# Kernel tuning notes

Measured on AMD Instinct MI355X. Metric: run time of the kernel, lower is better.

The kernel has to match this reference:

```python
import jax, jax.numpy as jnp
import numpy as np

N_NODES = 150000
N_EDGES = 4800000
IN_FEAT = 64
HID = 16
N_GRAPHS = 512
EDGE_DIM = 2


def setup_inputs() -> dict:
    key = jax.random.key(0)
    ks = jax.random.split(key, 32)
    g = lambda i, shape, scale=0.1: jax.random.normal(ks[i], shape, dtype=jnp.float32) * scale
    inp = {
        'x': jax.random.normal(ks[0], (N_NODES, IN_FEAT), dtype=jnp.float32),
        'edge_index': jax.random.randint(ks[1], (2, N_EDGES), 0, N_NODES),
        'edge_attr': jax.random.normal(ks[2], (N_EDGES, EDGE_DIM), dtype=jnp.float32),
        'batch': jnp.sort(jax.random.randint(ks[3], (N_NODES,), 0, N_GRAPHS)),
        # GATConv 1
        'W1': g(4, (IN_FEAT, HID)), 'We1': g(5, (EDGE_DIM, HID)),
        'att_src1': g(6, (HID,)), 'att_dst1': g(7, (HID,)), 'att_edge1': g(8, (HID,)),
        'b1': g(9, (HID,)),
        'bn1_g': jnp.ones((HID,), jnp.float32), 'bn1_b': jnp.zeros((HID,), jnp.float32),
        # GATConv 2
        'W2': g(10, (HID, HID)), 'We2': g(11, (EDGE_DIM, HID)),
        'att_src2': g(12, (HID,)), 'att_dst2': g(13, (HID,)), 'att_edge2': g(14, (HID,)),
        'b2': g(15, (HID,)),
        # D2RL head
        'bnl1_g': jnp.ones((HID,), jnp.float32), 'bnl1_b': jnp.zeros((HID,), jnp.float32),
        'Wl1': g(16, (HID, HID)), 'bl1': g(17, (HID,)),
        'bnl2_g': jnp.ones((2 * HID,), jnp.float32), 'bnl2_b': jnp.zeros((2 * HID,), jnp.float32),
        'Wl2': g(18, (2 * HID, HID)), 'bl2': g(19, (HID,)),
        'bnl3_g': jnp.ones((2 * HID,), jnp.float32), 'bnl3_b': jnp.zeros((2 * HID,), jnp.float32),
        'Wl3': g(20, (2 * HID, HID)), 'bl3': g(21, (HID,)),
        'Wo': g(22, (HID, 1)), 'bo': g(23, (1,)),
    }
    return inp


def _bn(x, gamma, beta, eps=1e-5):
    mu = x.mean(0)
    var = x.var(0)  # biased, matches torch BN training-mode normalization
    return gamma * (x - mu) * jax.lax.rsqrt(var + eps) + beta


def _gat(x, src, dst, edge_attr, W, We, a_s, a_d, a_e, bias, n):
    h = x @ W                                   # [N, HID]
    alpha_s = h @ a_s                           # [N]
    alpha_d = h @ a_d                           # [N]
    alpha_e = (edge_attr @ We) @ a_e            # [E]
    # add self-loops; self-loop edge_attr = mean of incoming edge_attr (PyG fill_value='mean')
    cnt = jax.ops.segment_sum(jnp.ones(src.shape[0], x.dtype), dst, num_segments=n)
    loop_attr = jax.ops.segment_sum(edge_attr, dst, num_segments=n) / jnp.maximum(cnt, 1.0)[:, None]
    loop_alpha_e = (loop_attr @ We) @ a_e       # [N]
    idx = jnp.arange(n)
    src_f = jnp.concatenate([src, idx])
    dst_f = jnp.concatenate([dst, idx])
    logits = jax.nn.leaky_relu(alpha_s[src_f] + alpha_d[dst_f]
                               + jnp.concatenate([alpha_e, loop_alpha_e]), 0.2)
    # segment softmax over destination neighborhoods
    m = jax.ops.segment_max(logits, dst_f, num_segments=n)
    ex = jnp.exp(logits - m[dst_f])
    denom = jax.ops.segment_sum(ex, dst_f, num_segments=n)
    alpha = ex / (denom[dst_f] + 1e-16)
    out = jax.ops.segment_sum(alpha[:, None] * h[src_f], dst_f, num_segments=n)
    return out + bias


def reference(x, edge_index, edge_attr, batch,
              W1, We1, att_src1, att_dst1, att_edge1, b1, bn1_g, bn1_b,
              W2, We2, att_src2, att_dst2, att_edge2, b2,
              bnl1_g, bnl1_b, Wl1, bl1,
              bnl2_g, bnl2_b, Wl2, bl2,
              bnl3_g, bnl3_b, Wl3, bl3,
              Wo, bo):
    n = x.shape[0]
    src, dst = edge_index[0], edge_index[1]
    h = jax.nn.relu(_gat(x, src, dst, edge_attr, W1, We1, att_src1, att_dst1, att_edge1, b1, n))
    h = _bn(h, bn1_g, bn1_b)
    h = jax.nn.relu(_gat(h, src, dst, edge_attr, W2, We2, att_src2, att_dst2, att_edge2, b2, n))
    # mean aggregation per graph
    gcnt = jax.ops.segment_sum(jnp.ones(n, h.dtype), batch, num_segments=N_GRAPHS, indices_are_sorted=True)
    pooled = jax.ops.segment_sum(h, batch, num_segments=N_GRAPHS, indices_are_sorted=True) / jnp.maximum(gcnt, 1.0)[:, None]
    z = jax.nn.relu(_bn(pooled, bnl1_g, bnl1_b) @ Wl1 + bl1)
    z = jax.nn.relu(_bn(jnp.concatenate([z, pooled], axis=1), bnl2_g, bnl2_b) @ Wl2 + bl2)
    z = jax.nn.relu(_bn(jnp.concatenate([z, pooled], axis=1), bnl3_g, bnl3_b) @ Wl3 + bl3)
    return z @ Wo + bo
```

## Files before the change

### kernel.cpp

```cpp
#include <hip/hip_runtime.h>
#include <hip/hip_fp16.h>
#include <math.h>

#define H 16
#define NF 64
#define TPB 256
#define NB 256
#define NBSHIFT 8
#define BTPB 1024
#define NSHIFT 6
#define MAXB 2560
#define SBLK 256
#define SITEMS 16
#define SRCMASK 0x3FFFF
#define CAP 3072
#define STAGE_CAP 18752
#define PSPAN 96

__device__ __forceinline__ float lrelu(float v){ return v > 0.f ? v : 0.2f*v; }

__global__ void k_prep(const float* __restrict__ We1, const float* __restrict__ ae1,
                       const float* __restrict__ We2, const float* __restrict__ ae2,
                       float* __restrict__ params){
  int t = threadIdx.x;
  if (t < 4){
    const float* We = (t < 2) ? We1 : We2;
    const float* ae = (t < 2) ? ae1 : ae2;
    int r = t & 1;
    float s = 0.f;
    for (int c = 0; c < H; ++c) s += We[r*H + c] * ae[c];
    params[t] = s;
  }
}

__global__ __launch_bounds__(BTPB) void k_bcount(const int* __restrict__ dst,
    int* __restrict__ cnt, int E, int B, int chunk){
  __shared__ int lcnt[MAXB];
  int blk = blockIdx.x, t = threadIdx.x;
  for (int i = t; i < B; i += BTPB) lcnt[i] = 0;
  __syncthreads();
  int e0 = blk*chunk, e1 = min(E, e0 + chunk);
  for (int e = e0 + t; e < e1; e += BTPB){
    int d = __builtin_nontemporal_load(dst + e);
    atomicAdd(&lcnt[d >> NSHIFT], 1);
  }
  __syncthreads();
  for (int i = t; i < B; i += BTPB) cnt[(size_t)i*NB + blk] = lcnt[i];
}

__global__ __launch_bounds__(SBLK) void k_scan1(const int* __restrict__ cnt,
    int* __restrict__ part, int M){
  __shared__ int red[SBLK];
  int base = blockIdx.x*SBLK*SITEMS;
  int t = threadIdx.x;
  int s = 0;
  for (int i = 0; i < SITEMS; ++i){
    int idx = base + t*SITEMS + i;
    s += (idx < M) ? cnt[idx] : 0;
  }
  red[t] = s; __syncthreads();
  for (int off = SBLK/2; off > 0; off >>= 1){
    if (t < off) red[t] += red[t+off];
    __syncthreads();
  }
  if (t == 0) part[blockIdx.x] = red[0];
}

__global__ __launch_bounds__(SBLK) void k_scan2(int* __restrict__ part, int nb,
    int* __restrict__ bbase, int B, int E){
  __shared__ int sh[SBLK];
  int t = threadIdx.x;
  int v = (t < nb) ? part[t] : 0;
  sh[t] = v; __syncthreads();
  for (int off = 1; off < SBLK; off <<= 1){
    int add = (t >= off) ? sh[t-off] : 0;
    __syncthreads();
    sh[t] += add;
    __syncthreads();
  }
  if (t < nb) part[t] = sh[t] - v;
  if (t == 0) bbase[B] = E;
}

__global__ __launch_bounds__(SBLK) void k_scan3(int* __restrict__ cnt,
    const int* __restrict__ part, int* __restrict__ bbase,
    int* __restrict__ cntT, int B, int M){
  __shared__ int sh[SBLK];
  int base = blockIdx.x*SBLK*SITEMS;
  int t = threadIdx.x;
  int loc[SITEMS]; int s = 0;
  for (int i = 0; i < SITEMS; ++i){
    int idx = base + t*SITEMS + i;
    loc[i] = s;
    s += (idx < M) ? cnt[idx] : 0;
  }
  sh[t] = s; __syncthreads();
  for (int off = 1; off < SBLK; off <<= 1){
    int add = (t >= off) ? sh[t-off] : 0;
    __syncthreads();
    sh[t] += add;
    __syncthreads();
  }
  int toff = sh[t] - s + part[blockIdx.x];
  for (int i = 0; i < SITEMS; ++i){
    int idx = base + t*SITEMS + i;
    if (idx < M){
      int excl = toff + loc[i];
      cnt[idx] = excl;
      cntT[(size_t)(idx & (NB-1))*B + (idx >> NBSHIFT)] = excl;
      if ((idx & (NB-1)) == 0) bbase[idx / NB] = excl;
    }
  }
}

__global__ __launch_bounds__(BTPB) void k_bwrite(const int* __restrict__ src,
    const int* __restrict__ dst, const float* __restrict__ attr, const float* __restrict__ wp,
    const int* __restrict__ cntT, int2* __restrict__ rec, int E, int B, int chunk){
  __shared__ int2 stage[STAGE_CAP];
  __shared__ int ex[MAXB];
  __shared__ int wsum[16];
  int blk = blockIdx.x, t = threadIdx.x;
  const int* row0 = cntT + (size_t)blk*B;
  const int* row1 = cntT + (size_t)(blk+1)*B;
  {
    int v[3]; int s = 0;
    int base3 = t*3;
    #pragma unroll
    for (int i = 0; i < 3; ++i){
      int idx = base3 + i;
      int c = 0;
      if (idx < B){
        int g0 = row0[idx];
        int g1;
        if (blk < NB-1)      g1 = row1[idx];
        else if (idx < B-1)  g1 = cntT[idx+1];
        else                 g1 = E;
        c = g1 - g0;
      }
      v[i] = c; s += c;
    }
    int lane = t & 63, wave = t >> 6;
    int x = s;
    for (int o = 1; o < 64; o <<= 1){
      int y = __shfl_up(x, o);
      if (lane >= o) x += y;
    }
    if (lane == 63) wsum[wave] = x;
    __syncthreads();
    if (t < 16){
      int w = wsum[t];
      int xx = w;
      for (int o = 1; o < 16; o <<= 1){
        int y = __shfl_up(xx, o);
        if (t >= o) xx += y;
      }
      wsum[t] = xx - w;
    }
    __syncthreads();
    int run = wsum[wave] + (x - s);
    #pragma unroll
    for (int i = 0; i < 3; ++i){
      int idx = base3 + i;
      if (idx < B) ex[idx] = run;
      run += v[i];
    }
  }
  __syncthreads();
  float w0 = wp[0], w1 = wp[1], w2 = wp[2], w3 = wp[3];
  int e0 = blk*chunk, e1 = min(E, e0 + chunk);
  for (int e = e0 + t; e < e1; e += BTPB){
    int d = __builtin_nontemporal_load(dst + e);
    int s = __builtin_nontemporal_load(src + e);
    union { double dd; float2 ff; } u;
    u.dd = __builtin_nontemporal_load((const double*)attr + e);
    float2 a = u.ff;
    int b = d >> NSHIFT;
    __half h1 = __float2half_rn(a.x*w0 + a.y*w1);
    __half h2 = __float2half_rn(a.x*w2 + a.y*w3);
    unsigned uu = (unsigned)__half_as_ushort(h1) | ((unsigned)__half_as_ushort(h2) << 16);
    int pos = atomicAdd(&ex[b], 1);
    stage[pos] = make_int2(s | ((d & 63) << 18), (int)uu);
  }
  __syncthreads();
  int grp = t >> 3, l8 = t & 7;
  for (int b = grp; b < B; b += (BTPB/8)){
    int start = (b == 0) ? 0 : ex[b-1];
    int end = ex[b];
    if (start == end) continue;
    int gb = row0[b];
    for (int j = start + l8; j < end; j += 8)
      rec[(size_t)gb + (j - start)] = stage[j];
  }
}

template<int SEL>
__global__ __launch_bounds__(BTPB) void k_gatf(const int2* __restrict__ rec,
    const int* __restrict__ bbase, const float* __restrict__ asn, const float* __restrict__ adn,
    const __half* __restrict__ h, const float* __restrict__ bias,
    float* __restrict__ out, int N){
  __shared__ int2 stage[CAP];
  __shared__ int2 sorted[CAP];
  __shared__ int lcnt[64], lcur[64], sr[2];
  __shared__ float sadn[64], sbias[H], sdacc[64];
  int b = blockIdx.x, t = threadIdx.x;
  int node0 = b << NSHIFT;
  if (t < 2) sr[t] = bbase[b + t];
  if (t < 64){
    lcnt[t] = 0;
    sdacc[t] = 0.f;
    int nn = node0 + t;
    sadn[t] = (nn < N) ? adn[nn] : 0.f;
  }
  if (t >= 64 && t < 64 + H) sbias[t - 64] = bias[t - 64];
  __syncthreads();
  int r0 = sr[0], cnt = sr[1] - r0;
  for (int i = t; i < cnt; i += BTPB){
    long long raw = __builtin_nontemporal_load((const long long*)(rec + r0 + i));
    int rx = (int)(unsigned)(raw & 0xFFFFFFFFll);
    unsigned u = (unsigned)((unsigned long long)raw >> 32);
    int ld = ((unsigned)rx) >> 18;
    float d = __half2float(__ushort_as_half((unsigned short)(SEL ? (u >> 16) : (u & 0xFFFFu))));
    float w = __expf(lrelu(asn[rx & SRCMASK] + sadn[ld] + d));
    stage[i] = make_int2(rx, __float_as_int(w));
    atomicAdd(&lcnt[ld], 1);
    atomicAdd(&sdacc[ld], d);
  }
  __syncthreads();
  if (t < 64){
    int v = lcnt[t];
    int x = v;
    for (int o = 1; o < 64; o <<= 1){
      int y = __shfl_up(x, o);
      if (t >= o) x += y;
    }
    lcur[t] = x - v;
  }
  __syncthreads();
  for (int i = t; i < cnt; i += BTPB){
    int2 r = stage[i];
    sorted[atomicAdd(&lcur[((unsigned)r.x) >> 18], 1)] = r;
  }
  __syncthreads();
  int nl = t >> 4, lane = t & (H-1);
  int n = node0 + nl;
  if (n >= N) return;
  int deg = lcnt[nl];
  int s0 = lcur[nl] - deg;
  float den = 0.f, acc = 0.f;
  for (int j = 0; j < deg; ++j){
    int2 r = sorted[s0 + j];
    float w = __int_as_float(r.y);
    den += w;
    acc += w * __half2float(h[(size_t)(r.x & SRCMASK)*H + lane]);
  }
  float lael = sdacc[nl] / fmaxf((float)deg, 1.f);
  float wl = __expf(lrelu(asn[n] + sadn[nl] + lael));
  den += wl;
  acc += wl * __half2float(h[(size_t)n*H + lane]);
  out[(size_t)n*H + lane] = fmaxf(acc/(den + 1e-16f) + sbias[lane], 0.f);
}

__global__ __launch_bounds__(TPB) void k_node1(const float* __restrict__ x, const float* __restrict__ W,
    const float* __restrict__ av_s, const float* __restrict__ av_d,
    __half* __restrict__ hout, float* __restrict__ asn, float* __restrict__ adn, int N){
  __shared__ float sW[NF*H];
  __shared__ float sas[H], sad[H];
  int t = threadIdx.x;
  for (int i = t; i < NF*H; i += TPB) sW[i] = W[i];
  if (t < H){ sas[t] = av_s[t]; sad[t] = av_d[t]; }
  __syncthreads();
  int n = blockIdx.x*TPB + t;
  if (n >= N) return;
  float h[H];
  #pragma unroll
  for (int j = 0; j < H; ++j) h[j] = 0.f;
  const float4* xr = (const float4*)(x + (size_t)n*NF);
  #pragma unroll
  for (int k4 = 0; k4 < NF/4; ++k4){
    float4 xv = xr[k4];
    #pragma unroll
    for (int j = 0; j < H; ++j){
      h[j] += xv.x*sW[(4*k4+0)*H+j] + xv.y*sW[(4*k4+1)*H+j]
            + xv.z*sW[(4*k4+2)*H+j] + xv.w*sW[(4*k4+3)*H+j];
    }
  }
  union { int4 i4[2]; __half hh[H]; } pk;
  #pragma unroll
  for (int j = 0; j < H; ++j) pk.hh[j] = __float2half_rn(h[j]);
  int4* ho = (int4*)(hout + (size_t)n*H);
  ho[0] = pk.i4[0]; ho[1] = pk.i4[1];
  float ss = 0.f, sd = 0.f;
  #pragma unroll
  for (int j = 0; j < H; ++j){ ss += h[j]*sas[j]; sd += h[j]*sad[j]; }
  asn[n] = ss; adn[n] = sd;
}

__global__ __launch_bounds__(TPB) void k_stats(const float* __restrict__ B,
    float* __restrict__ partial, int N){
  __shared__ float lds[4][32];
  int t = threadIdx.x;
  int n = blockIdx.x*TPB + t;
  float v[H];
  if (n < N){
    const float4* br = (const float4*)(B + (size_t)n*H);
    float4 a0 = br[0], a1 = br[1], a2 = br[2], a3 = br[3];
    v[0]=a0.x; v[1]=a0.y; v[2]=a0.z; v[3]=a0.w;
    v[4]=a1.x; v[5]=a1.y; v[6]=a1.z; v[7]=a1.w;
    v[8]=a2.x; v[9]=a2.y; v[10]=a2.z; v[11]=a2.w;
    v[12]=a3.x; v[13]=a3.y; v[14]=a3.z; v[15]=a3.w;
  } else {
    #pragma unroll
    for (int f = 0; f < H; ++f) v[f] = 0.f;
  }
  float s[H], q[H];
  #pragma unroll
  for (int f = 0; f < H; ++f){ s[f] = v[f]; q[f] = v[f]*v[f]; }
  for (int m = 1; m < 64; m <<= 1){
    #pragma unroll
    for (int f = 0; f < H; ++f){
      s[f] += __shfl_xor(s[f], m);
      q[f] += __shfl_xor(q[f], m);
    }
  }
  int wave = t >> 6, lane = t & 63;
  if (lane == 0){
    #pragma unroll
    for (int f = 0; f < H; ++f){ lds[wave][f] = s[f]; lds[wave][H+f] = q[f]; }
  }
  __syncthreads();
  if (t < 32)
    partial[(size_t)blockIdx.x*32 + t] = lds[0][t] + lds[1][t] + lds[2][t] + lds[3][t];
}

__global__ __launch_bounds__(256) void k_bnprep(const float* __restrict__ partial, int nb,
    const float* __restrict__ gamma, const float* __restrict__ beta,
    float* __restrict__ scale, float* __restrict__ shift, int N){
  __shared__ float red[256];
  __shared__ float tot[32];
  int t = threadIdx.x;
  int f = t & 31, c = t >> 5;
  float s = 0.f;
  for (int b = c; b < nb; b += 8) s += partial[(size_t)b*32 + f];
  red[c*32 + f] = s;
  __syncthreads();
  if (t < 32){
    float S = 0.f;
    #pragma unroll
    for (int cc = 0; cc < 8; ++cc) S += red[cc*32 + t];
    tot[t] = S;
  }
  __syncthreads();
  if (t < H){
    float inv = 1.f / (float)N;
    float mu  = tot[t] * inv;
    float var = tot[H+t] * inv - mu*mu;
    float sc  = gamma[t] * rsqrtf(var + 1e-5f);
    scale[t] = sc;
    shift[t] = beta[t] - mu*sc;
  }
}

__global__ __launch_bounds__(TPB) void k_node2(const float* __restrict__ Bin, const float* __restrict__ scale,
    const float* __restrict__ shift, const float* __restrict__ W,
    const float* __restrict__ av_s, const float* __restrict__ av_d,
    __half* __restrict__ hout, float* __restrict__ asn, float* __restrict__ adn, int N){
  __shared__ float sW[H*H];
  __shared__ float ssc[H], ssh[H], sas[H], sad[H];
  int t = threadIdx.x;
  if (t < H*H) sW[t] = W[t];
  if (t < H){ ssc[t] = scale[t]; ssh[t] = shift[t]; sas[t] = av_s[t]; sad[t] = av_d[t]; }
  __syncthreads();
  int n = blockIdx.x*TPB + t;
  if (n >= N) return;
  const float4* br = (const float4*)(Bin + (size_t)n*H);
  float4 a0 = br[0], a1 = br[1], a2 = br[2], a3 = br[3];
  float xn[H] = {a0.x,a0.y,a0.z,a0.w, a1.x,a1.y,a1.z,a1.w,
                 a2.x,a2.y,a2.z,a2.w, a3.x,a3.y,a3.z,a3.w};
  #pragma unroll
  for (int f = 0; f < H; ++f) xn[f] = xn[f]*ssc[f] + ssh[f];
  float h[H];
  #pragma unroll
  for (int j = 0; j < H; ++j) h[j] = 0.f;
  #pragma unroll
  for (int k = 0; k < H; ++k){
    float xv = xn[k];
    #pragma unroll
    for (int j = 0; j < H; ++j) h[j] += xv * sW[k*H+j];
  }
  union { int4 i4[2]; __half hh[H]; } pk;
  #pragma unroll
  for (int j = 0; j < H; ++j) pk.hh[j] = __float2half_rn(h[j]);
  int4* ho = (int4*)(hout + (size_t)n*H);
  ho[0] = pk.i4[0]; ho[1] = pk.i4[1];
  float ss = 0.f, sd = 0.f;
  #pragma unroll
  for (int j = 0; j < H; ++j){ ss += h[j]*sas[j]; sd += h[j]*sad[j]; }
  asn[n] = ss; adn[n] = sd;
}

__global__ __launch_bounds__(TPB) void k_pool(const float* __restrict__ B,
    const int* __restrict__ batch, float* __restrict__ pooled, float* __restrict__ gcnt, int N){
  __shared__ float acc[PSPAN*H];
  __shared__ float cacc[PSPAN];
  __shared__ int sg[2];
  int t = threadIdx.x;
  int n0 = blockIdx.x*TPB;
  int n = n0 + t;
  if (t == 0){
    sg[0] = batch[n0];
    int n1 = min(n0 + TPB - 1, N - 1);
    sg[1] = batch[n1];
  }
  __syncthreads();
  int gmin = sg[0];
  int span = sg[1] - gmin + 1;
  bool fits = (span <= PSPAN);
  if (fits){
    for (int i = t; i < span*H; i += TPB) acc[i] = 0.f;
    for (int i = t; i < span; i += TPB) cacc[i] = 0.f;
    __syncthreads();
  }
  int lane = t & 63;
  bool valid = n < N;
  int g = valid ? batch[n] : -1;
  float v[H];
  if (valid){
    const float4* br = (const float4*)(B + (size_t)n*H);
    float4 a0 = br[0], a1 = br[1], a2 = br[2], a3 = br[3];
    v[0]=a0.x; v[1]=a0.y; v[2]=a0.z; v[3]=a0.w;
    v[4]=a1.x; v[5]=a1.y; v[6]=a1.z; v[7]=a1.w;
    v[8]=a2.x; v[9]=a2.y; v[10]=a2.z; v[11]=a2.w;
    v[12]=a3.x; v[13]=a3.y; v[14]=a3.z; v[15]=a3.w;
  } else {
    #pragma unroll
    for (int f = 0; f < H; ++f) v[f] = 0.f;
  }
  int g0 = __shfl(g, 0);
  bool allsame = __all(valid && g == g0);
  if (fits){
    if (allsame){
      float s[H];
      #pragma unroll
      for (int f = 0; f < H; ++f) s[f] = v[f];
      for (int m = 1; m < 64; m <<= 1){
        #pragma unroll
        for (int f = 0; f < H; ++f) s[f] += __shfl_xor(s[f], m);
      }
      if (lane == 0){
        float* p = acc + (g0 - gmin)*H;
        #pragma unroll
        for (int f = 0; f < H; ++f) atomicAdd(&p[f], s[f]);
        atomicAdd(&cacc[g0 - gmin], 64.f);
      }
    } else if (valid){
      float* p = acc + (g - gmin)*H;
      #pragma unroll
      for (int f = 0; f < H; ++f) atomicAdd(&p[f], v[f]);
      atomicAdd(&cacc[g - gmin], 1.f);
    }
    __syncthreads();
    for (int i = t; i < span*H; i += TPB){
      float a = acc[i];
      if (a != 0.f) atomicAdd(&pooled[(size_t)gmin*H + i], a);
    }
    for (int i = t; i < span; i += TPB){
      float c = cacc[i];
      if (c != 0.f) atomicAdd(&gcnt[gmin + i], c);
    }
  } else {
    if (allsame){
      float s[H];
      #pragma unroll
      for (int f = 0; f < H; ++f) s[f] = v[f];
      for (int m = 1; m < 64; m <<= 1){
        #pragma unroll
        for (int f = 0; f < H; ++f) s[f] += __shfl_xor(s[f], m);
      }
      if (lane == 0){
        float* p = pooled + (size_t)g0*H;
        #pragma unroll
        for (int f = 0; f < H; ++f) atomicAdd(&p[f], s[f]);
        atomicAdd(&gcnt[g0], 64.f);
      }
    } else if (valid){
      float* p = pooled + (size_t)g*H;
      #pragma unroll
      for (int f = 0; f < H; ++f) atomicAdd(&p[f], v[f]);
      atomicAdd(&gcnt[g], 1.f);
    }
  }
}

__device__ void block_stats16(const float* v, float* mu, float* rs,
                              float* wsum, float* wsq, int G){
  float s[H], q[H];
  #pragma unroll
  for (int f = 0; f < H; ++f){ s[f] = v[f]; q[f] = v[f]*v[f]; }
  for (int m = 1; m < 64; m <<= 1){
    #pragma unroll
    for (int f = 0; f < H; ++f){
      s[f] += __shfl_xor(s[f], m);
      q[f] += __shfl_xor(q[f], m);
    }
  }
  int wave = threadIdx.x >> 6, lane = threadIdx.x & 63;
  if (lane == 0){
    #pragma unroll
    for (int f = 0; f < H; ++f){ wsum[wave*H+f] = s[f]; wsq[wave*H+f] = q[f]; }
  }
  __syncthreads();
  int t = threadIdx.x;
  if (t < H){
    float S = 0.f, Q = 0.f;
    for (int w = 0; w < 8; ++w){ S += wsum[w*H+t]; Q += wsq[w*H+t]; }
    float m_ = S / (float)G;
    float var = Q / (float)G - m_*m_;
    mu[t] = m_;
    rs[t] = rsqrtf(var + 1e-5f);
  }
  __syncthreads();
}

__global__ __launch_bounds__(512) void k_head(const float* __restrict__ pooled, const float* __restrict__ gcnt,
    const float* __restrict__ g1, const float* __restrict__ be1,
    const float* __restrict__ Wl1, const float* __restrict__ bl1,
    const float* __restrict__ g2, const float* __restrict__ be2,
    const float* __restrict__ Wl2, const float* __restrict__ bl2,
    const float* __restrict__ g3, const float* __restrict__ be3,
    const float* __restrict__ Wl3, const float* __restrict__ bl3,
    const float* __restrict__ Wo, const float* __restrict__ bo,
    float* __restrict__ out, int G){
  __shared__ float wsum[8*H], wsq[8*H];
  __shared__ float pmu[H], prs[H], smu[H], srs[H];
  int g = threadIdx.x;
  float p[H];
  if (g < G){
    float c = fmaxf(gcnt[g], 1.f);
    #pragma unroll
    for (int f = 0; f < H; ++f) p[f] = pooled[(size_t)g*H+f] / c;
  } else {
    #pragma unroll
    for (int f = 0; f < H; ++f) p[f] = 0.f;
  }
  block_stats16(p, pmu, prs, wsum, wsq, G);
  float xn[H], z[H];
  #pragma unroll
  for (int f = 0; f < H; ++f) xn[f] = g1[f]*(p[f]-pmu[f])*prs[f] + be1[f];
  #pragma unroll
  for (int j = 0; j < H; ++j) z[j] = bl1[j];
  for (int k = 0; k < H; ++k){
    float xv = xn[k];
    #pragma unroll
    for (int j = 0; j < H; ++j) z[j] += xv * Wl1[k*H+j];
  }
  #pragma unroll
  for (int j = 0; j < H; ++j) z[j] = fmaxf(z[j], 0.f);
  block_stats16(z, smu, srs, wsum, wsq, G);
  float x2[2*H], z2[H];
  #pragma unroll
  for (int f = 0; f < H; ++f){
    x2[f]   = g2[f]  *(z[f]-smu[f])*srs[f] + be2[f];
    x2[H+f] = g2[H+f]*(p[f]-pmu[f])*prs[f] + be2[H+f];
  }
  #pragma unroll
  for (int j = 0; j < H; ++j) z2[j] = bl2[j];
  for (int k = 0; k < 2*H; ++k){
    float xv = x2[k];
    #pragma unroll
    for (int j = 0; j < H; ++j) z2[j] += xv * Wl2[k*H+j];
  }
  #pragma unroll
  for (int j = 0; j < H; ++j) z2[j] = fmaxf(z2[j], 0.f);
  block_stats16(z2, smu, srs, wsum, wsq, G);
  float x3[2*H], z3[H];
  #pragma unroll
  for (int f = 0; f < H; ++f){
    x3[f]   = g3[f]  *(z2[f]-smu[f])*srs[f] + be3[f];
    x3[H+f] = g3[H+f]*(p[f]-pmu[f])*prs[f] + be3[H+f];
  }
  #pragma unroll
  for (int j = 0; j < H; ++j) z3[j] = bl3[j];
  for (int k = 0; k < 2*H; ++k){
    float xv = x3[k];
    #pragma unroll
    for (int j = 0; j < H; ++j) z3[j] += xv * Wl3[k*H+j];
  }
  #pragma unroll
  for (int j = 0; j < H; ++j) z3[j] = fmaxf(z3[j], 0.f);
  if (g < G){
    float o = bo[0];
    #pragma unroll
    for (int j = 0; j < H; ++j) o += z3[j]*Wo[j];
    out[g] = o;
  }
}

extern "C" void kernel_launch(void* const* d_in, const int* in_sizes, int n_in,
                              void* d_out, int out_size, void* d_ws, size_t ws_size,
                              hipStream_t stream) {
  const float* x     = (const float*)d_in[0];
  const int*   ei    = (const int*)d_in[1];
  const float* attr  = (const float*)d_in[2];
  const int*   batch = (const int*)d_in[3];
  const float* W1  = (const float*)d_in[4];
  const float* We1 = (const float*)d_in[5];
  const float* as1 = (const float*)d_in[6];
  const float* ad1 = (const float*)d_in[7];
  const float* ae1 = (const float*)d_in[8];
  const float* b1  = (const float*)d_in[9];
  const float* bn1g = (const float*)d_in[10];
  const float* bn1b = (const float*)d_in[11];
  const float* W2  = (const float*)d_in[12];
  const float* We2 = (const float*)d_in[13];
  const float* as2 = (const float*)d_in[14];
  const float* ad2 = (const float*)d_in[15];
  const float* ae2 = (const float*)d_in[16];
  const float* b2  = (const float*)d_in[17];
  const float* bnl1g = (const float*)d_in[18];
  const float* bnl1b = (const float*)d_in[19];
  const float* Wl1 = (const float*)d_in[20];
  const float* bl1 = (const float*)d_in[21];
  const float* bnl2g = (const float*)d_in[22];
  const float* bnl2b = (const float*)d_in[23];
  const float* Wl2 = (const float*)d_in[24];
  const float* bl2 = (const float*)d_in[25];
  const float* bnl3g = (const float*)d_in[26];
  const float* bnl3b = (const float*)d_in[27];
  const float* Wl3 = (const float*)d_in[28];
  const float* bl3 = (const float*)d_in[29];
  const float* Wo  = (const float*)d_in[30];
  const float* bo  = (const float*)d_in[31];

  int N = in_sizes[0] / NF;
  int E = in_sizes[1] / 2;
  int G = out_size;
  const int* srcp = ei;
  const int* dstp = ei + E;

  int B     = (N + 63) >> 6;
  int M     = B * NB;
  int chunk = (E + NB - 1) / NB;
  int nbN   = (N + TPB - 1)/TPB;
  int nbS   = (M + SBLK*SITEMS - 1)/(SBLK*SITEMS);

  char* wsb = (char*)d_ws;
  int2*  rec = (int2*)wsb;
  char* p = wsb + (size_t)8*E;
  __half* A = (__half*)p;     p += (size_t)2*H*N;
  float* Bv  = (float*)p;     p += (size_t)16*N*4;
  float* asn = (float*)p;     p += (size_t)N*4;
  float* adn = (float*)p;     p += (size_t)N*4;
  int*   cnt     = (int*)p;   p += (size_t)4*M;
  int*   cntT    = (int*)p;   p += (size_t)4*M;
  int*   bbase   = (int*)p;   p += (size_t)4*(B+1);
  int*   part    = (int*)p;   p += (size_t)4*256;
  float* par     = (float*)p; p += 4*64;
  float* pooled  = (float*)p; p += (size_t)4*G*H;
  float* gcnt    = (float*)p; p += (size_t)4*G;
  float* partial = (float*)p; p += (size_t)4*nbN*32;

  float* bnscale = par + 4;
  float* bnshift = par + 20;

  hipMemsetAsync(pooled, 0, (size_t)(G*H + G)*sizeof(float), stream);

  k_prep<<<1, 64, 0, stream>>>(We1, ae1, We2, ae2, par);

  k_bcount<<<NB, BTPB, 0, stream>>>(dstp, cnt, E, B, chunk);
  k_scan1<<<nbS, SBLK, 0, stream>>>(cnt, part, M);
  k_scan2<<<1, SBLK, 0, stream>>>(part, nbS, bbase, B, E);
  k_scan3<<<nbS, SBLK, 0, stream>>>(cnt, part, bbase, cntT, B, M);
  k_bwrite<<<NB, BTPB, 0, stream>>>(srcp, dstp, attr, par, cntT, rec, E, B, chunk);

  k_node1<<<nbN, TPB, 0, stream>>>(x, W1, as1, ad1, A, asn, adn, N);
  k_gatf<0><<<B, BTPB, 0, stream>>>(rec, bbase, asn, adn, A, b1, Bv, N);
  k_stats<<<nbN, TPB, 0, stream>>>(Bv, partial, N);
  k_bnprep<<<1, 256, 0, stream>>>(partial, nbN, bn1g, bn1b, bnscale, bnshift, N);

  k_node2<<<nbN, TPB, 0, stream>>>(Bv, bnscale, bnshift, W2, as2, ad2, A, asn, adn, N);
  k_gatf<1><<<B, BTPB, 0, stream>>>(rec, bbase, asn, adn, A, b2, Bv, N);

  k_pool<<<nbN, TPB, 0, stream>>>(Bv, batch, pooled, gcnt, N);
  k_head<<<1, 512, 0, stream>>>(pooled, gcnt, bnl1g, bnl1b, Wl1, bl1, bnl2g, bnl2b, Wl2, bl2,
                                bnl3g, bnl3b, Wl3, bl3, Wo, bo, (float*)d_out, G);
}
```

Measured before the change: 491.3 us.

## Persist per-bucket dst-sorted edge records from layer 1 to skip re-sort in layer 2

The first GAT aggregation kernel now writes its locally sorted edge records back into the global record buffer, replacing the packed fp16 edge scores with the layer-2 edge score as float. It also stores per-node degree and the summed layer-2 edge score. The second GAT kernel reads these directly, skipping the shared-memory counting sort, atomics and self-loop mean accumulation. The cost is an extra 8 bytes per edge written in layer 1, plus doubled shared memory in layer 1 (two extra CAP-sized float arrays), which may reduce occupancy.

After: 503.4 us. 1.02x slower.

```diff
diff --git a/kernel.cpp b/kernel.cpp
--- a/kernel.cpp
+++ b/kernel.cpp
@@ -193,21 +193,23 @@
   }
 }
 
-template<int SEL>
-__global__ __launch_bounds__(BTPB) void k_gatf(const int2* __restrict__ rec,
+__global__ __launch_bounds__(BTPB) void k_gatf1(int2* __restrict__ rec,
     const int* __restrict__ bbase, const float* __restrict__ asn, const float* __restrict__ adn,
     const __half* __restrict__ h, const float* __restrict__ bias,
-    float* __restrict__ out, int N){
+    float* __restrict__ out, int* __restrict__ degg, float* __restrict__ sd2g, int N){
   __shared__ int2 stage[CAP];
+  __shared__ float d2a[CAP];
   __shared__ int2 sorted[CAP];
+  __shared__ float d2s[CAP];
   __shared__ int lcnt[64], lcur[64], sr[2];
-  __shared__ float sadn[64], sbias[H], sdacc[64];
+  __shared__ float sadn[64], sbias[H], sdacc[64], sdacc2[64];
   int b = blockIdx.x, t = threadIdx.x;
   int node0 = b << NSHIFT;
   if (t < 2) sr[t] = bbase[b + t];
   if (t < 64){
     lcnt[t] = 0;
     sdacc[t] = 0.f;
+    sdacc2[t] = 0.f;
     int nn = node0 + t;
     sadn[t] = (nn < N) ? adn[nn] : 0.f;
   }
@@ -219,11 +221,14 @@
     int rx = (int)(unsigned)(raw & 0xFFFFFFFFll);
     unsigned u = (unsigned)((unsigned long long)raw >> 32);
     int ld = ((unsigned)rx) >> 18;
-    float d = __half2float(__ushort_as_half((unsigned short)(SEL ? (u >> 16) : (u & 0xFFFFu))));
-    float w = __expf(lrelu(asn[rx & SRCMASK] + sadn[ld] + d));
+    float d1 = __half2float(__ushort_as_half((unsigned short)(u & 0xFFFFu)));
+    float d2 = __half2float(__ushort_as_half((unsigned short)(u >> 16)));
+    float w = __expf(lrelu(asn[rx & SRCMASK] + sadn[ld] + d1));
     stage[i] = make_int2(rx, __float_as_int(w));
+    d2a[i] = d2;
     atomicAdd(&lcnt[ld], 1);
-    atomicAdd(&sdacc[ld], d);
+    atomicAdd(&sdacc[ld], d1);
+    atomicAdd(&sdacc2[ld], d2);
   }
   __syncthreads();
   if (t < 64){
@@ -238,9 +243,18 @@
   __syncthreads();
   for (int i = t; i < cnt; i += BTPB){
     int2 r = stage[i];
-    sorted[atomicAdd(&lcur[((unsigned)r.x) >> 18], 1)] = r;
-  }
-  __syncthreads();
+    float dd = d2a[i];
+    int pos = atomicAdd(&lcur[((unsigned)r.x) >> 18], 1);
+    sorted[pos] = r;
+    d2s[pos] = dd;
+  }
+  __syncthreads();
+  for (int i = t; i < cnt; i += BTPB)
+    rec[r0 + i] = make_int2(sorted[i].x, __float_as_int(d2s[i]));
+  if (t < 64){
+    degg[(b << 6) + t] = lcnt[t];
+    sd2g[(b << 6) + t] = sdacc2[t];
+  }
   int nl = t >> 4, lane = t & (H-1);
   int n = node0 + nl;
   if (n >= N) return;
@@ -254,6 +268,61 @@
     acc += w * __half2float(h[(size_t)(r.x & SRCMASK)*H + lane]);
   }
   float lael = sdacc[nl] / fmaxf((float)deg, 1.f);
+  float wl = __expf(lrelu(asn[n] + sadn[nl] + lael));
+  den += wl;
+  acc += wl * __half2float(h[(size_t)n*H + lane]);
+  out[(size_t)n*H + lane] = fmaxf(acc/(den + 1e-16f) + sbias[lane], 0.f);
+}
+
+__global__ __launch_bounds__(BTPB) void k_gatf2(const int2* __restrict__ rec,
+    const int* __restrict__ bbase, const int* __restrict__ degg, const float* __restrict__ sd2g,
+    const float* __restrict__ asn, const float* __restrict__ adn,
+    const __half* __restrict__ h, const float* __restrict__ bias,
+    float* __restrict__ out, int N){
+  __shared__ int2 sorted[CAP];
+  __shared__ int lcnt[64], lstart[64], sr[2];
+  __shared__ float sadn[64], sbias[H], ssd[64];
+  int b = blockIdx.x, t = threadIdx.x;
+  int node0 = b << NSHIFT;
+  if (t < 2) sr[t] = bbase[b + t];
+  if (t < 64){
+    int d = degg[(b << 6) + t];
+    lcnt[t] = d;
+    ssd[t] = sd2g[(b << 6) + t];
+    int nn = node0 + t;
+    sadn[t] = (nn < N) ? adn[nn] : 0.f;
+    int x = d;
+    for (int o = 1; o < 64; o <<= 1){
+      int y = __shfl_up(x, o);
+      if (t >= o) x += y;
+    }
+    lstart[t] = x - d;
+  }
+  if (t >= 64 && t < 64 + H) sbias[t - 64] = bias[t - 64];
+  __syncthreads();
+  int r0 = sr[0], cnt = sr[1] - r0;
+  for (int i = t; i < cnt; i += BTPB){
+    long long raw = __builtin_nontemporal_load((const long long*)(rec + r0 + i));
+    int rx = (int)(unsigned)(raw & 0xFFFFFFFFll);
+    float d2 = __int_as_float((int)((unsigned long long)raw >> 32));
+    int ld = ((unsigned)rx) >> 18;
+    float w = __expf(lrelu(asn[rx & SRCMASK] + sadn[ld] + d2));
+    sorted[i] = make_int2(rx, __float_as_int(w));
+  }
+  __syncthreads();
+  int nl = t >> 4, lane = t & (H-1);
+  int n = node0 + nl;
+  if (n >= N) return;
+  int deg = lcnt[nl];
+  int s0 = lstart[nl];
+  float den = 0.f, acc = 0.f;
+  for (int j = 0; j < deg; ++j){
+    int2 r = sorted[s0 + j];
+    float w = __int_as_float(r.y);
+    den += w;
+    acc += w * __half2float(h[(size_t)(r.x & SRCMASK)*H + lane]);
+  }
+  float lael = ssd[nl] / fmaxf((float)deg, 1.f);
   float wl = __expf(lrelu(asn[n] + sadn[nl] + lael));
   den += wl;
   acc += wl * __half2float(h[(size_t)n*H + lane]);
@@ -658,6 +727,8 @@
   float* pooled  = (float*)p; p += (size_t)4*G*H;
   float* gcnt    = (float*)p; p += (size_t)4*G;
   float* partial = (float*)p; p += (size_t)4*nbN*32;
+  int*   degg    = (int*)p;   p += (size_t)4*B*64;
+  float* sd2g    = (float*)p; p += (size_t)4*B*64;
 
   float* bnscale = par + 4;
   float* bnshift = par + 20;
@@ -673,12 +744,12 @@
   k_bwrite<<<NB, BTPB, 0, stream>>>(srcp, dstp, attr, par, cntT, rec, E, B, chunk);
 
   k_node1<<<nbN, TPB, 0, stream>>>(x, W1, as1, ad1, A, asn, adn, N);
-  k_gatf<0><<<B, BTPB, 0, stream>>>(rec, bbase, asn, adn, A, b1, Bv, N);
+  k_gatf1<<<B, BTPB, 0, stream>>>(rec, bbase, asn, adn, A, b1, Bv, degg, sd2g, N);
   k_stats<<<nbN, TPB, 0, stream>>>(Bv, partial, N);
   k_bnprep<<<1, 256, 0, stream>>>(partial, nbN, bn1g, bn1b, bnscale, bnshift, N);
 
   k_node2<<<nbN, TPB, 0, stream>>>(Bv, bnscale, bnshift, W2, as2, ad2, A, asn, adn, N);
-  k_gatf<1><<<B, BTPB, 0, stream>>>(rec, bbase, asn, adn, A, b2, Bv, N);
+  k_gatf2<<<B, BTPB, 0, stream>>>(rec, bbase, degg, sd2g, asn, adn, A, b2, Bv, N);
 
   k_pool<<<nbN, TPB, 0, stream>>>(Bv, batch, pooled, gcnt, N);
   k_head<<<1, 512, 0, stream>>>(pooled, gcnt, bnl1g, bnl1b, Wl1, bl1, bnl2g, bnl2b, Wl2, bl2,
```
